# Kernel tuning notes

Measured on AMD Instinct MI355X. Metric: run time of the kernel, lower is better.

The kernel has to match this reference:

```python
import jax, jax.numpy as jnp
import numpy as np

N_CLASSES = 256
N_AUDIO_CHANS = 1
N_CHANS = 128
N_RES = 128
N_SKIP = 256
N_END = 256
KERNEL = 2
N_LAYERS = 10
N_STACKS = 3
DILATIONS = [2 ** i for _ in range(N_STACKS) for i in range(N_LAYERS)]
L = len(DILATIONS)
DN = ('NCW', 'OIW', 'NCW')


def setup_inputs() -> dict:
    key = jax.random.key(0)
    ks = jax.random.split(key, 16)
    s = 0.05  # small init keeps 30-layer residual stack numerically tame
    inp = {
        'x': jax.random.normal(ks[0], (4, N_AUDIO_CHANS, 16384), jnp.float32),
        'w_shift': jax.random.normal(ks[1], (N_CHANS, N_AUDIO_CHANS, KERNEL), jnp.float32) * s,
        'b_shift': jnp.zeros((N_CHANS,), jnp.float32),
        'conv_w': jax.random.normal(ks[2], (L, 2 * N_RES, N_CHANS, KERNEL), jnp.float32) * s,
        'conv_b': jnp.zeros((L, 2 * N_RES), jnp.float32),
        'res_w': jax.random.normal(ks[3], (L, N_CHANS, N_RES), jnp.float32) * s,
        'res_b': jnp.zeros((L, N_CHANS), jnp.float32),
        'skip_w': jax.random.normal(ks[4], (L, N_SKIP, N_RES), jnp.float32) * s,
        'skip_b': jnp.zeros((L, N_SKIP), jnp.float32),
        'a_w': jax.random.normal(ks[5], (N_END, N_SKIP), jnp.float32) * s,
        'a_b': jnp.zeros((N_END,), jnp.float32),
        'b_w': jax.random.normal(ks[6], (N_CLASSES * N_AUDIO_CHANS, N_END), jnp.float32) * s,
        'b_b': jnp.zeros((N_CLASSES * N_AUDIO_CHANS,), jnp.float32),
    }
    return inp


def _causal_conv(x, w, b, dilation):
    # left-pad by (k-1)*dilation so outputs depend only on past/present
    pad = (w.shape[-1] - 1) * dilation
    xp = jnp.pad(x, ((0, 0), (0, 0), (pad, 0)))
    y = jax.lax.conv_general_dilated(xp, w, window_strides=(1,), padding='VALID',
                                     rhs_dilation=(dilation,), dimension_numbers=DN)
    return y + b[None, :, None]


def reference(x, w_shift, b_shift, conv_w, conv_b, res_w, res_b,
              skip_w, skip_b, a_w, a_b, b_w, b_b):
    N, C, W = x.shape
    # shifted conv: shift input right by one (prepend 0, drop last), then causal conv
    xs = jnp.pad(x, ((0, 0), (0, 0), (1, 0)))[:, :, :-1]
    h = _causal_conv(xs, w_shift, b_shift, 1)  # (N, n_chans, W)

    skips = jnp.zeros((N, N_SKIP, W), h.dtype)
    for l in range(L):
        g = _causal_conv(h, conv_w[l], conv_b[l], DILATIONS[l])  # (N, 2*res, W)
        a, b_gate = jnp.split(g, 2, axis=1)
        gated = a * jax.nn.sigmoid(b_gate)                        # GLU, (N, res, W)
        h = jnp.einsum('or,nrw->now', res_w[l], gated) + res_b[l][None, :, None] + h
        skips = skips + jnp.einsum('or,nrw->now', skip_w[l], gated) + skip_b[l][None, :, None]

    z = jax.nn.relu(skips)
    z = jax.nn.relu(jnp.einsum('os,nsw->now', a_w, z) + a_b[None, :, None])
    logits = jnp.einsum('oe,new->now', b_w, z) + b_b[None, :, None]
    return logits.reshape(N, N_CLASSES, N_AUDIO_CHANS, W)
```

## Files before the change

### kernel.cpp

```cpp
#include <hip/hip_runtime.h>
#include <math.h>


#define NB 4
#define WLEN 16384
#define C 128
#define S 256
#define NLAYERS 30
#define TT 64
#define NTB (WLEN / TT)
#define XROW 264
#define GROW 136

typedef _Float16 half8 __attribute__((ext_vector_type(8)));
typedef _Float16 half4 __attribute__((ext_vector_type(4)));
typedef float floatx4 __attribute__((ext_vector_type(4)));

__device__ __forceinline__ float sigmoidf_(float v) {
    return 1.0f / (1.0f + __expf(-v));
}

__global__ void prep_kernel(const float* __restrict__ conv_w,
                            const float* __restrict__ res_w,
                            const float* __restrict__ skip_w,
                            const float* __restrict__ a_w,
                            const float* __restrict__ b_w,
                            const float* __restrict__ conv_b,
                            const float* __restrict__ skip_b,
                            _Float16* __restrict__ cw,
                            _Float16* __restrict__ rsw,
                            _Float16* __restrict__ skw,
                            _Float16* __restrict__ aw,
                            _Float16* __restrict__ bw,
                            float* __restrict__ cbp,
                            float* __restrict__ ssum) {
    const int ncw = NLAYERS * 256 * 256;
    const int nrs = NLAYERS * 128 * 128;
    const int nsk = NLAYERS * 256 * 128;
    const int nab = 256 * 256;
    const int ncb = NLAYERS * 256;
    const int total = ncw + nrs + nsk + nab + nab + ncb + 256;
    for (int idx = blockIdx.x * blockDim.x + threadIdx.x; idx < total;
         idx += gridDim.x * blockDim.x) {
        int i = idx;
        if (i < ncw) {
            int j = i & 7, lane = (i >> 3) & 63, rest = i >> 9;
            int ks = rest & 7; rest >>= 3;
            int mt = rest & 15; int l = rest >> 4;
            int mp = mt * 16 + (lane & 15);
            int orow = (mp >> 1) + (mp & 1) * 128;
            int k = ks * 32 + (lane >> 4) * 8 + j;
            int tap = k >> 7, c = k & 127;
            cw[i] = (_Float16)conv_w[(((size_t)l * 256 + orow) * 128 + c) * 2 + tap];
        } else if (i < ncw + nrs) {
            i -= ncw;
            int j = i & 7, lane = (i >> 3) & 63, rest = i >> 9;
            int ks = rest & 3; rest >>= 2;
            int mt = rest & 7; int l = rest >> 3;
            int m = mt * 16 + (lane & 15);
            int k = ks * 32 + (lane >> 4) * 8 + j;
            rsw[i] = (_Float16)res_w[((size_t)l * 128 + m) * 128 + k];
        } else if (i < ncw + nrs + nsk) {
            i -= ncw + nrs;
            int j = i & 7, lane = (i >> 3) & 63, rest = i >> 9;
            int ks = rest & 3; rest >>= 2;
            int mt = rest & 15; int l = rest >> 4;
            int m = mt * 16 + (lane & 15);
            int k = ks * 32 + (lane >> 4) * 8 + j;
            skw[i] = (_Float16)skip_w[((size_t)l * 256 + m) * 128 + k];
        } else if (i < ncw + nrs + nsk + nab) {
            i -= ncw + nrs + nsk;
            int j = i & 7, lane = (i >> 3) & 63, rest = i >> 9;
            int ks = rest & 7; int mt = rest >> 3;
            aw[i] = (_Float16)a_w[(mt * 16 + (lane & 15)) * 256 + ks * 32 + (lane >> 4) * 8 + j];
        } else if (i < ncw + nrs + nsk + 2 * nab) {
            i -= ncw + nrs + nsk + nab;
            int j = i & 7, lane = (i >> 3) & 63, rest = i >> 9;
            int ks = rest & 7; int mt = rest >> 3;
            bw[i] = (_Float16)b_w[(mt * 16 + (lane & 15)) * 256 + ks * 32 + (lane >> 4) * 8 + j];
        } else if (i < ncw + nrs + nsk + 2 * nab + ncb) {
            i -= ncw + nrs + nsk + 2 * nab;
            int mp = i & 255; int l = i >> 8;
            cbp[i] = conv_b[l * 256 + (mp >> 1) + (mp & 1) * 128];
        } else {
            i -= ncw + nrs + nsk + 2 * nab + ncb;
            float s = 0.f;
            for (int l = 0; l < NLAYERS; ++l) s += skip_b[l * 256 + i];
            ssum[i] = s;
        }
    }
}

__global__ void front_kernel(const float* __restrict__ x,
                             const float* __restrict__ w_shift,
                             const float* __restrict__ b_shift,
                             _Float16* __restrict__ h) {
    const int n = blockIdx.y;
    const int t = blockIdx.x * 256 + threadIdx.x;
    float x1 = (t >= 1) ? x[n * WLEN + t - 1] : 0.0f;
    float x2 = (t >= 2) ? x[n * WLEN + t - 2] : 0.0f;
    _Float16* hq = h + ((size_t)n * WLEN + t) * 128;
    #pragma unroll
    for (int c0 = 0; c0 < 128; c0 += 8) {
        half8 v;
        #pragma unroll
        for (int j = 0; j < 8; ++j) {
            int c = c0 + j;
            v[j] = (_Float16)fmaf(w_shift[2 * c], x2,
                                  fmaf(w_shift[2 * c + 1], x1, b_shift[c]));
        }
        *(half8*)&hq[c0] = v;
    }
}

template <bool FIRST>
__global__ __launch_bounds__(256, 4) void layer_kernel(
    const _Float16* __restrict__ h_in, _Float16* __restrict__ h_out,
    _Float16* __restrict__ chunk,
    const _Float16* __restrict__ cw, const float* __restrict__ cb,
    const _Float16* __restrict__ rsw, const float* __restrict__ rb,
    const _Float16* __restrict__ skw, const float* __restrict__ ssum, int d) {
    __shared__ _Float16 SMEM[2 * TT * GROW];
    _Float16* X0 = SMEM;
    _Float16* X1 = SMEM + TT * GROW;
    _Float16* G  = X0;
    const int n = blockIdx.y, tb = blockIdx.x, t0 = tb * TT;
    const int tid = threadIdx.x;
    const int wave = __builtin_amdgcn_readfirstlane(tid >> 6);
    const int lane = tid & 63, q = lane >> 4, ml = lane & 15;

    const _Float16* hn = h_in + (size_t)n * WLEN * 128;
    #pragma unroll
    for (int it = 0; it < 8; ++it) {
        int idx = it * 256 + tid;
        int seg = idx & 15;
        int rowc = (idx >> 4) & 63;
        int tap = idx >> 10;
        int src_t = t0 + rowc - (tap ? 0 : d);
        half8 v = (half8)(_Float16)0.0f;
        if (src_t >= 0)
            v = *(const half8*)&hn[(size_t)src_t * 128 + seg * 8];
        _Float16* Xb = tap ? X1 : X0;
        *(half8*)&Xb[rowc * GROW + seg * 8] = v;
    }
    __syncthreads();

    floatx4 acc[4][4];
    #pragma unroll
    for (int mt = 0; mt < 4; ++mt)
        #pragma unroll
        for (int r = 0; r < 4; ++r) {
            float bias = cb[64 * wave + mt * 16 + q * 4 + r];
            #pragma unroll
            for (int nt = 0; nt < 4; ++nt) acc[mt][nt][r] = bias;
        }
    #pragma unroll
    for (int half = 0; half < 2; ++half) {
        const _Float16* Xb = half ? X1 : X0;
        for (int ks = 0; ks < 4; ++ks) {
            half8 b[4];
            #pragma unroll
            for (int nt = 0; nt < 4; ++nt)
                b[nt] = *(const half8*)&Xb[(nt * 16 + ml) * GROW + ks * 32 + q * 8];
            #pragma unroll
            for (int mt = 0; mt < 4; ++mt) {
                half8 a = *(const half8*)&cw[((((4 * wave + mt) * 8) + half * 4 + ks) * 64 + lane) * 8];
                #pragma unroll
                for (int nt = 0; nt < 4; ++nt)
                    acc[mt][nt] = __builtin_amdgcn_mfma_f32_16x16x32_f16(a, b[nt], acc[mt][nt], 0, 0, 0);
            }
        }
    }
    __syncthreads();

    #pragma unroll
    for (int mt = 0; mt < 4; ++mt)
        #pragma unroll
        for (int nt = 0; nt < 4; ++nt) {
            float g0 = acc[mt][nt][0] * sigmoidf_(acc[mt][nt][1]);
            float g1 = acc[mt][nt][2] * sigmoidf_(acc[mt][nt][3]);
            _Float16 p[2] = {(_Float16)g0, (_Float16)g1};
            *(uint32_t*)&G[(nt * 16 + ml) * GROW + 32 * wave + mt * 8 + 2 * q] = *(uint32_t*)p;
        }
    __syncthreads();

    {
        floatx4 sacc[4][4];
        #pragma unroll
        for (int mt = 0; mt < 4; ++mt)
            #pragma unroll
            for (int r = 0; r < 4; ++r) {
                float bias = FIRST ? ssum[64 * wave + mt * 16 + q * 4 + r] : 0.0f;
                #pragma unroll
                for (int nt = 0; nt < 4; ++nt) sacc[mt][nt][r] = bias;
            }
        #pragma unroll
        for (int ks = 0; ks < 4; ++ks) {
            half8 b[4];
            #pragma unroll
            for (int nt = 0; nt < 4; ++nt)
                b[nt] = *(const half8*)&G[(nt * 16 + ml) * GROW + ks * 32 + q * 8];
            #pragma unroll
            for (int mt = 0; mt < 4; ++mt) {
                half8 a = *(const half8*)&skw[((((4 * wave + mt) * 4) + ks) * 64 + lane) * 8];
                #pragma unroll
                for (int nt = 0; nt < 4; ++nt)
                    sacc[mt][nt] = __builtin_amdgcn_mfma_f32_16x16x32_f16(a, b[nt], sacc[mt][nt], 0, 0, 0);
            }
        }
        _Float16* cp = chunk + ((size_t)n * NTB + tb) * 16384;
        #pragma unroll
        for (int mt = 0; mt < 4; ++mt)
            #pragma unroll
            for (int nt = 0; nt < 4; ++nt) {
                size_t o = (size_t)((((wave * 4 + mt) * 4) + nt) * 64 + lane) * 4;
                if (FIRST) {
                    half4 v;
                    #pragma unroll
                    for (int r = 0; r < 4; ++r) v[r] = (_Float16)sacc[mt][nt][r];
                    *(half4*)&cp[o] = v;
                } else {
                    half4 v = *(const half4*)&cp[o];
                    half4 w;
                    #pragma unroll
                    for (int r = 0; r < 4; ++r)
                        w[r] = (_Float16)(sacc[mt][nt][r] + (float)v[r]);
                    *(half4*)&cp[o] = w;
                }
            }
    }

    {
        floatx4 racc[2][4];
        #pragma unroll
        for (int mt = 0; mt < 2; ++mt)
            #pragma unroll
            for (int r = 0; r < 4; ++r) {
                float bias = rb[32 * wave + mt * 16 + q * 4 + r];
                #pragma unroll
                for (int nt = 0; nt < 4; ++nt) racc[mt][nt][r] = bias;
            }
        #pragma unroll
        for (int ks = 0; ks < 4; ++ks) {
            half8 b[4];
            #pragma unroll
            for (int nt = 0; nt < 4; ++nt)
                b[nt] = *(const half8*)&G[(nt * 16 + ml) * GROW + ks * 32 + q * 8];
            #pragma unroll
            for (int mt = 0; mt < 2; ++mt) {
                half8 a = *(const half8*)&rsw[((((2 * wave + mt) * 4) + ks) * 64 + lane) * 8];
                #pragma unroll
                for (int nt = 0; nt < 4; ++nt)
                    racc[mt][nt] = __builtin_amdgcn_mfma_f32_16x16x32_f16(a, b[nt], racc[mt][nt], 0, 0, 0);
            }
        }
        _Float16* ho = h_out + (size_t)n * WLEN * 128;
        #pragma unroll
        for (int mt = 0; mt < 2; ++mt)
            #pragma unroll
            for (int nt = 0; nt < 4; ++nt) {
                int tt = nt * 16 + ml;
                int c = 32 * wave + mt * 16 + q * 4;
                half4 hv = *(const half4*)&X1[tt * GROW + c];
                half4 o;
                #pragma unroll
                for (int r = 0; r < 4; ++r)
                    o[r] = (_Float16)(racc[mt][nt][r] + (float)hv[r]);
                *(half4*)&ho[(size_t)(t0 + tt) * 128 + c] = o;
            }
    }
}

__global__ __launch_bounds__(256, 4) void head_kernel(
    float* __restrict__ out, const _Float16* __restrict__ chunk,
    const _Float16* __restrict__ aw, const float* __restrict__ ab,
    const _Float16* __restrict__ bw, const float* __restrict__ bb) {
    __shared__ _Float16 X[TT * XROW];
    const int n = blockIdx.y, tb = blockIdx.x, t0 = tb * TT;
    const int tid = threadIdx.x;
    const int wave = __builtin_amdgcn_readfirstlane(tid >> 6);
    const int lane = tid & 63, q = lane >> 4, ml = lane & 15;

    {
        const _Float16* cp = chunk + ((size_t)n * NTB + tb) * 16384;
        #pragma unroll
        for (int mt = 0; mt < 4; ++mt)
            #pragma unroll
            for (int nt = 0; nt < 4; ++nt) {
                size_t o = (size_t)((((wave * 4 + mt) * 4) + nt) * 64 + lane) * 4;
                half4 v = *(const half4*)&cp[o];
                half4 z;
                #pragma unroll
                for (int r = 0; r < 4; ++r)
                    z[r] = (_Float16)fmaxf((float)v[r], 0.0f);
                *(half4*)&X[(nt * 16 + ml) * XROW + 64 * wave + mt * 16 + q * 4] = z;
            }
    }
    __syncthreads();

    floatx4 acc[4][4];
    #pragma unroll
    for (int mt = 0; mt < 4; ++mt)
        #pragma unroll
        for (int r = 0; r < 4; ++r) {
            float bias = ab[64 * wave + mt * 16 + q * 4 + r];
            #pragma unroll
            for (int nt = 0; nt < 4; ++nt) acc[mt][nt][r] = bias;
        }
    for (int ks = 0; ks < 8; ++ks) {
        half8 b[4];
        #pragma unroll
        for (int nt = 0; nt < 4; ++nt)
            b[nt] = *(const half8*)&X[(nt * 16 + ml) * XROW + ks * 32 + q * 8];
        #pragma unroll
        for (int mt = 0; mt < 4; ++mt) {
            half8 a = *(const half8*)&aw[((((4 * wave + mt) * 8) + ks) * 64 + lane) * 8];
            #pragma unroll
            for (int nt = 0; nt < 4; ++nt)
                acc[mt][nt] = __builtin_amdgcn_mfma_f32_16x16x32_f16(a, b[nt], acc[mt][nt], 0, 0, 0);
        }
    }
    __syncthreads();
    #pragma unroll
    for (int mt = 0; mt < 4; ++mt)
        #pragma unroll
        for (int nt = 0; nt < 4; ++nt) {
            half4 z;
            #pragma unroll
            for (int r = 0; r < 4; ++r)
                z[r] = (_Float16)fmaxf(acc[mt][nt][r], 0.0f);
            *(half4*)&X[(nt * 16 + ml) * XROW + 64 * wave + mt * 16 + q * 4] = z;
        }
    __syncthreads();

    #pragma unroll
    for (int mt = 0; mt < 4; ++mt)
        #pragma unroll
        for (int r = 0; r < 4; ++r) {
            float bias = bb[64 * wave + mt * 16 + q * 4 + r];
            #pragma unroll
            for (int nt = 0; nt < 4; ++nt) acc[mt][nt][r] = bias;
        }
    for (int ks = 0; ks < 8; ++ks) {
        half8 b[4];
        #pragma unroll
        for (int nt = 0; nt < 4; ++nt)
            b[nt] = *(const half8*)&X[(nt * 16 + ml) * XROW + ks * 32 + q * 8];
        #pragma unroll
        for (int mt = 0; mt < 4; ++mt) {
            half8 a = *(const half8*)&bw[((((4 * wave + mt) * 8) + ks) * 64 + lane) * 8];
            #pragma unroll
            for (int nt = 0; nt < 4; ++nt)
                acc[mt][nt] = __builtin_amdgcn_mfma_f32_16x16x32_f16(a, b[nt], acc[mt][nt], 0, 0, 0);
        }
    }
    float* on = out + (size_t)n * S * WLEN;
    #pragma unroll
    for (int mt = 0; mt < 4; ++mt)
        #pragma unroll
        for (int nt = 0; nt < 4; ++nt)
            #pragma unroll
            for (int r = 0; r < 4; ++r) {
                int o = 64 * wave + mt * 16 + q * 4 + r;
                int tt = t0 + nt * 16 + ml;
                on[(size_t)o * WLEN + tt] = acc[mt][nt][r];
            }
}

extern "C" void kernel_launch(void* const* d_in, const int* in_sizes, int n_in,
                              void* d_out, int out_size, void* d_ws, size_t ws_size,
                              hipStream_t stream) {
    (void)in_sizes; (void)n_in; (void)out_size; (void)ws_size;
    const float* x       = (const float*)d_in[0];
    const float* w_shift = (const float*)d_in[1];
    const float* b_shift = (const float*)d_in[2];
    const float* conv_w  = (const float*)d_in[3];
    const float* conv_b  = (const float*)d_in[4];
    const float* res_w   = (const float*)d_in[5];
    const float* res_b   = (const float*)d_in[6];
    const float* skip_w  = (const float*)d_in[7];
    const float* skip_b  = (const float*)d_in[8];
    const float* a_w     = (const float*)d_in[9];
    const float* a_b     = (const float*)d_in[10];
    const float* b_w     = (const float*)d_in[11];
    const float* b_b     = (const float*)d_in[12];
    float* out = (float*)d_out;

    char* ws = (char*)d_ws;
    size_t off = 0;
    _Float16* hA    = (_Float16*)(ws + off); off += (size_t)NB * WLEN * 128 * 2;
    _Float16* hB    = (_Float16*)(ws + off); off += (size_t)NB * WLEN * 128 * 2;
    _Float16* chunk = (_Float16*)(ws + off); off += (size_t)NB * NTB * 16384 * 2;
    _Float16* cw  = (_Float16*)(ws + off); off += (size_t)NLAYERS * 256 * 256 * 2;
    _Float16* rsw = (_Float16*)(ws + off); off += (size_t)NLAYERS * 128 * 128 * 2;
    _Float16* skw = (_Float16*)(ws + off); off += (size_t)NLAYERS * 256 * 128 * 2;
    _Float16* aw  = (_Float16*)(ws + off); off += 256 * 256 * 2;
    _Float16* bw  = (_Float16*)(ws + off); off += 256 * 256 * 2;
    float* cbp  = (float*)(ws + off); off += (size_t)NLAYERS * 256 * 4;
    float* ssum = (float*)(ws + off); off += 256 * 4;

    prep_kernel<<<512, 256, 0, stream>>>(conv_w, res_w, skip_w, a_w, b_w,
                                         conv_b, skip_b,
                                         cw, rsw, skw, aw, bw, cbp, ssum);
    front_kernel<<<dim3(WLEN / 256, NB), 256, 0, stream>>>(x, w_shift, b_shift, hA);

    const dim3 grid(NTB, NB);
    _Float16* hin = hA;
    _Float16* hout = hB;
    for (int l = 0; l < NLAYERS; ++l) {
        int dil = 1 << (l % 10);
        const _Float16* cwp = cw + (size_t)l * 65536;
        const _Float16* rsp = rsw + (size_t)l * 16384;
        const _Float16* skp = skw + (size_t)l * 32768;
        if (l == 0)
            layer_kernel<true><<<grid, 256, 0, stream>>>(
                hin, hout, chunk, cwp, cbp + l * 256,
                rsp, res_b + l * 128, skp, ssum, dil);
        else
            layer_kernel<false><<<grid, 256, 0, stream>>>(
                hin, hout, chunk, cwp, cbp + l * 256,
                rsp, res_b + l * 128, skp, ssum, dil);
        _Float16* tmp = hin; hin = hout; hout = tmp;
    }

    head_kernel<<<grid, 256, 0, stream>>>(out, chunk, aw, a_b, bw, b_b);
}
```

Baseline: 1.150 ms.

## Fuse all WaveNet layers and head into one persistent cooperative kernel

Replaces the 30 per-layer launches and the head launch with a single cooperative kernel that loops over layers and uses a grid-wide sync between them. Skip accumulators stay in registers as fp16 across layers, so the chunk buffer round-trip through global memory is no longer needed. The head is fused at the end. The cost is a grid barrier per layer, higher register pressure from the persistent skip state, and fp16 rounding of the skip sum after every layer. If the occupancy check fails, the old multi-kernel path is used instead.

```diff
diff --git a/kernel.cpp b/kernel.cpp
--- a/kernel.cpp
+++ b/kernel.cpp
@@ -1,5 +1,8 @@
 #include <hip/hip_runtime.h>
+#include <hip/hip_cooperative_groups.h>
 #include <math.h>
+
+namespace cg = cooperative_groups;
 
 
 #define NB 4
@@ -113,6 +116,272 @@
     }
 }
 
+__global__ __launch_bounds__(256, 4) void wavenet_coop(
+    _Float16* __restrict__ hA, _Float16* __restrict__ hB,
+    float* __restrict__ out,
+    const _Float16* __restrict__ cw_all, const float* __restrict__ cbp_all,
+    const _Float16* __restrict__ rsw_all, const float* __restrict__ rb_all,
+    const _Float16* __restrict__ skw_all, const float* __restrict__ ssum,
+    const _Float16* __restrict__ aw, const float* __restrict__ ab,
+    const _Float16* __restrict__ bw, const float* __restrict__ bb) {
+    __shared__ _Float16 SMEM[2 * TT * GROW];
+    _Float16* X0 = SMEM;
+    _Float16* X1 = SMEM + TT * GROW;
+    _Float16* G  = X0;
+    cg::grid_group gg = cg::this_grid();
+    const int n = blockIdx.y, tb = blockIdx.x, t0 = tb * TT;
+    const int tid = threadIdx.x;
+    const int wave = __builtin_amdgcn_readfirstlane(tid >> 6);
+    const int lane = tid & 63, q = lane >> 4, ml = lane & 15;
+
+    half4 sk16[4][4];
+
+    #pragma clang loop unroll(disable)
+    for (int l = 0; l < NLAYERS; ++l) {
+        const _Float16* hin = (l & 1) ? hB : hA;
+        _Float16* hout      = (l & 1) ? hA : hB;
+        const int d = 1 << (l % 10);
+        const _Float16* cw  = cw_all  + (size_t)l * 65536;
+        const float*    cb  = cbp_all + l * 256;
+        const _Float16* rsw = rsw_all + (size_t)l * 16384;
+        const float*    rb  = rb_all  + l * 128;
+        const _Float16* skw = skw_all + (size_t)l * 32768;
+
+        const _Float16* hn = hin + (size_t)n * WLEN * 128;
+        #pragma unroll
+        for (int it = 0; it < 8; ++it) {
+            int idx = it * 256 + tid;
+            int seg = idx & 15;
+            int rowc = (idx >> 4) & 63;
+            int tap = idx >> 10;
+            int src_t = t0 + rowc - (tap ? 0 : d);
+            half8 v = (half8)(_Float16)0.0f;
+            if (src_t >= 0)
+                v = *(const half8*)&hn[(size_t)src_t * 128 + seg * 8];
+            _Float16* Xb = tap ? X1 : X0;
+            *(half8*)&Xb[rowc * GROW + seg * 8] = v;
+        }
+        __syncthreads();
+
+        uint32_t glu[4][4];
+        #pragma unroll
+        for (int mp2 = 0; mp2 < 2; ++mp2) {
+            floatx4 acc[2][4];
+            #pragma unroll
+            for (int i = 0; i < 2; ++i) {
+                int mt = 2 * mp2 + i;
+                #pragma unroll
+                for (int r = 0; r < 4; ++r) {
+                    float bias = cb[64 * wave + mt * 16 + q * 4 + r];
+                    #pragma unroll
+                    for (int nt = 0; nt < 4; ++nt) acc[i][nt][r] = bias;
+                }
+            }
+            #pragma unroll
+            for (int hp = 0; hp < 2; ++hp) {
+                const _Float16* Xb = hp ? X1 : X0;
+                for (int ks = 0; ks < 4; ++ks) {
+                    half8 b[4];
+                    #pragma unroll
+                    for (int nt = 0; nt < 4; ++nt)
+                        b[nt] = *(const half8*)&Xb[(nt * 16 + ml) * GROW + ks * 32 + q * 8];
+                    #pragma unroll
+                    for (int i = 0; i < 2; ++i) {
+                        int mt = 2 * mp2 + i;
+                        half8 a = *(const half8*)&cw[((((4 * wave + mt) * 8) + hp * 4 + ks) * 64 + lane) * 8];
+                        #pragma unroll
+                        for (int nt = 0; nt < 4; ++nt)
+                            acc[i][nt] = __builtin_amdgcn_mfma_f32_16x16x32_f16(a, b[nt], acc[i][nt], 0, 0, 0);
+                    }
+                }
+            }
+            #pragma unroll
+            for (int i = 0; i < 2; ++i)
+                #pragma unroll
+                for (int nt = 0; nt < 4; ++nt) {
+                    float g0 = acc[i][nt][0] * sigmoidf_(acc[i][nt][1]);
+                    float g1 = acc[i][nt][2] * sigmoidf_(acc[i][nt][3]);
+                    _Float16 p[2] = {(_Float16)g0, (_Float16)g1};
+                    glu[2 * mp2 + i][nt] = *(uint32_t*)p;
+                }
+        }
+        __syncthreads();
+        #pragma unroll
+        for (int mt = 0; mt < 4; ++mt)
+            #pragma unroll
+            for (int nt = 0; nt < 4; ++nt)
+                *(uint32_t*)&G[(nt * 16 + ml) * GROW + 32 * wave + mt * 8 + 2 * q] = glu[mt][nt];
+        __syncthreads();
+
+        {
+            floatx4 sacc[4][4];
+            if (l == 0) {
+                #pragma unroll
+                for (int mt = 0; mt < 4; ++mt)
+                    #pragma unroll
+                    for (int r = 0; r < 4; ++r) {
+                        float bias = ssum[64 * wave + mt * 16 + q * 4 + r];
+                        #pragma unroll
+                        for (int nt = 0; nt < 4; ++nt) sacc[mt][nt][r] = bias;
+                    }
+            } else {
+                #pragma unroll
+                for (int mt = 0; mt < 4; ++mt)
+                    #pragma unroll
+                    for (int nt = 0; nt < 4; ++nt)
+                        #pragma unroll
+                        for (int r = 0; r < 4; ++r)
+                            sacc[mt][nt][r] = (float)sk16[mt][nt][r];
+            }
+            #pragma unroll
+            for (int ks = 0; ks < 4; ++ks) {
+                half8 b[4];
+                #pragma unroll
+                for (int nt = 0; nt < 4; ++nt)
+                    b[nt] = *(const half8*)&G[(nt * 16 + ml) * GROW + ks * 32 + q * 8];
+                #pragma unroll
+                for (int mt = 0; mt < 4; ++mt) {
+                    half8 a = *(const half8*)&skw[((((4 * wave + mt) * 4) + ks) * 64 + lane) * 8];
+                    #pragma unroll
+                    for (int nt = 0; nt < 4; ++nt)
+                        sacc[mt][nt] = __builtin_amdgcn_mfma_f32_16x16x32_f16(a, b[nt], sacc[mt][nt], 0, 0, 0);
+                }
+            }
+            #pragma unroll
+            for (int mt = 0; mt < 4; ++mt)
+                #pragma unroll
+                for (int nt = 0; nt < 4; ++nt)
+                    #pragma unroll
+                    for (int r = 0; r < 4; ++r)
+                        sk16[mt][nt][r] = (_Float16)sacc[mt][nt][r];
+        }
+
+        if (l != NLAYERS - 1) {
+            floatx4 racc[2][4];
+            #pragma unroll
+            for (int mt = 0; mt < 2; ++mt)
+                #pragma unroll
+                for (int r = 0; r < 4; ++r) {
+                    float bias = rb[32 * wave + mt * 16 + q * 4 + r];
+                    #pragma unroll
+                    for (int nt = 0; nt < 4; ++nt) racc[mt][nt][r] = bias;
+                }
+            #pragma unroll
+            for (int ks = 0; ks < 4; ++ks) {
+                half8 b[4];
+                #pragma unroll
+                for (int nt = 0; nt < 4; ++nt)
+                    b[nt] = *(const half8*)&G[(nt * 16 + ml) * GROW + ks * 32 + q * 8];
+                #pragma unroll
+                for (int mt = 0; mt < 2; ++mt) {
+                    half8 a = *(const half8*)&rsw[((((2 * wave + mt) * 4) + ks) * 64 + lane) * 8];
+                    #pragma unroll
+                    for (int nt = 0; nt < 4; ++nt)
+                        racc[mt][nt] = __builtin_amdgcn_mfma_f32_16x16x32_f16(a, b[nt], racc[mt][nt], 0, 0, 0);
+                }
+            }
+            _Float16* ho = hout + (size_t)n * WLEN * 128;
+            #pragma unroll
+            for (int mt = 0; mt < 2; ++mt)
+                #pragma unroll
+                for (int nt = 0; nt < 4; ++nt) {
+                    int tt = nt * 16 + ml;
+                    int c = 32 * wave + mt * 16 + q * 4;
+                    half4 hv = *(const half4*)&X1[tt * GROW + c];
+                    half4 o;
+                    #pragma unroll
+                    for (int r = 0; r < 4; ++r)
+                        o[r] = (_Float16)(racc[mt][nt][r] + (float)hv[r]);
+                    *(half4*)&ho[(size_t)(t0 + tt) * 128 + c] = o;
+                }
+            gg.sync();
+        }
+    }
+
+    __syncthreads();
+    _Float16* X = SMEM;
+    #pragma unroll
+    for (int mt = 0; mt < 4; ++mt)
+        #pragma unroll
+        for (int nt = 0; nt < 4; ++nt) {
+            half4 v = sk16[mt][nt];
+            half4 z;
+            #pragma unroll
+            for (int r = 0; r < 4; ++r)
+                z[r] = (_Float16)fmaxf((float)v[r], 0.0f);
+            *(half4*)&X[(nt * 16 + ml) * XROW + 64 * wave + mt * 16 + q * 4] = z;
+        }
+    __syncthreads();
+
+    floatx4 acc[4][4];
+    #pragma unroll
+    for (int mt = 0; mt < 4; ++mt)
+        #pragma unroll
+        for (int r = 0; r < 4; ++r) {
+            float bias = ab[64 * wave + mt * 16 + q * 4 + r];
+            #pragma unroll
+            for (int nt = 0; nt < 4; ++nt) acc[mt][nt][r] = bias;
+        }
+    for (int ks = 0; ks < 8; ++ks) {
+        half8 b[4];
+        #pragma unroll
+        for (int nt = 0; nt < 4; ++nt)
+            b[nt] = *(const half8*)&X[(nt * 16 + ml) * XROW + ks * 32 + q * 8];
+        #pragma unroll
+        for (int mt = 0; mt < 4; ++mt) {
+            half8 a = *(const half8*)&aw[((((4 * wave + mt) * 8) + ks) * 64 + lane) * 8];
+            #pragma unroll
+            for (int nt = 0; nt < 4; ++nt)
+                acc[mt][nt] = __builtin_amdgcn_mfma_f32_16x16x32_f16(a, b[nt], acc[mt][nt], 0, 0, 0);
+        }
+    }
+    __syncthreads();
+    #pragma unroll
+    for (int mt = 0; mt < 4; ++mt)
+        #pragma unroll
+        for (int nt = 0; nt < 4; ++nt) {
+            half4 z;
+            #pragma unroll
+            for (int r = 0; r < 4; ++r)
+                z[r] = (_Float16)fmaxf(acc[mt][nt][r], 0.0f);
+            *(half4*)&X[(nt * 16 + ml) * XROW + 64 * wave + mt * 16 + q * 4] = z;
+        }
+    __syncthreads();
+
+    #pragma unroll
+    for (int mt = 0; mt < 4; ++mt)
+        #pragma unroll
+        for (int r = 0; r < 4; ++r) {
+            float bias = bb[64 * wave + mt * 16 + q * 4 + r];
+            #pragma unroll
+            for (int nt = 0; nt < 4; ++nt) acc[mt][nt][r] = bias;
+        }
+    for (int ks = 0; ks < 8; ++ks) {
+        half8 b[4];
+        #pragma unroll
+        for (int nt = 0; nt < 4; ++nt)
+            b[nt] = *(const half8*)&X[(nt * 16 + ml) * XROW + ks * 32 + q * 8];
+        #pragma unroll
+        for (int mt = 0; mt < 4; ++mt) {
+            half8 a = *(const half8*)&bw[((((4 * wave + mt) * 8) + ks) * 64 + lane) * 8];
+            #pragma unroll
+            for (int nt = 0; nt < 4; ++nt)
+                acc[mt][nt] = __builtin_amdgcn_mfma_f32_16x16x32_f16(a, b[nt], acc[mt][nt], 0, 0, 0);
+        }
+    }
+    float* on = out + (size_t)n * S * WLEN;
+    #pragma unroll
+    for (int mt = 0; mt < 4; ++mt)
+        #pragma unroll
+        for (int nt = 0; nt < 4; ++nt)
+            #pragma unroll
+            for (int r = 0; r < 4; ++r) {
+                int o = 64 * wave + mt * 16 + q * 4 + r;
+                int tt = t0 + nt * 16 + ml;
+                on[(size_t)o * WLEN + tt] = acc[mt][nt][r];
+            }
+}
+
 template <bool FIRST>
 __global__ __launch_bounds__(256, 4) void layer_kernel(
     const _Float16* __restrict__ h_in, _Float16* __restrict__ h_out,
@@ -155,8 +424,8 @@
             for (int nt = 0; nt < 4; ++nt) acc[mt][nt][r] = bias;
         }
     #pragma unroll
-    for (int half = 0; half < 2; ++half) {
-        const _Float16* Xb = half ? X1 : X0;
+    for (int hp = 0; hp < 2; ++hp) {
+        const _Float16* Xb = hp ? X1 : X0;
         for (int ks = 0; ks < 4; ++ks) {
             half8 b[4];
             #pragma unroll
@@ -164,7 +433,7 @@
                 b[nt] = *(const half8*)&Xb[(nt * 16 + ml) * GROW + ks * 32 + q * 8];
             #pragma unroll
             for (int mt = 0; mt < 4; ++mt) {
-                half8 a = *(const half8*)&cw[((((4 * wave + mt) * 8) + half * 4 + ks) * 64 + lane) * 8];
+                half8 a = *(const half8*)&cw[((((4 * wave + mt) * 8) + hp * 4 + ks) * 64 + lane) * 8];
                 #pragma unroll
                 for (int nt = 0; nt < 4; ++nt)
                     acc[mt][nt] = __builtin_amdgcn_mfma_f32_16x16x32_f16(a, b[nt], acc[mt][nt], 0, 0, 0);
@@ -405,23 +674,42 @@
     front_kernel<<<dim3(WLEN / 256, NB), 256, 0, stream>>>(x, w_shift, b_shift, hA);
 
     const dim3 grid(NTB, NB);
-    _Float16* hin = hA;
-    _Float16* hout = hB;
-    for (int l = 0; l < NLAYERS; ++l) {
-        int dil = 1 << (l % 10);
-        const _Float16* cwp = cw + (size_t)l * 65536;
-        const _Float16* rsp = rsw + (size_t)l * 16384;
-        const _Float16* skp = skw + (size_t)l * 32768;
-        if (l == 0)
-            layer_kernel<true><<<grid, 256, 0, stream>>>(
-                hin, hout, chunk, cwp, cbp + l * 256,
-                rsp, res_b + l * 128, skp, ssum, dil);
-        else
-            layer_kernel<false><<<grid, 256, 0, stream>>>(
-                hin, hout, chunk, cwp, cbp + l * 256,
-                rsp, res_b + l * 128, skp, ssum, dil);
-        _Float16* tmp = hin; hin = hout; hout = tmp;
-    }
-
-    head_kernel<<<grid, 256, 0, stream>>>(out, chunk, aw, a_b, bw, b_b);
+
+    static int coop_blocks_per_cu = -1;
+    if (coop_blocks_per_cu < 0) {
+        int nb = 0;
+        if (hipOccupancyMaxActiveBlocksPerMultiprocessor(&nb, wavenet_coop, 256, 0)
+            != hipSuccess)
+            nb = 0;
+        coop_blocks_per_cu = nb;
+    }
+
+    bool launched = false;
+    if (coop_blocks_per_cu >= 4) {
+        void* args[] = {&hA, &hB, &out, &cw, &cbp, &rsw, (void*)&res_b,
+                        &skw, &ssum, &aw, (void*)&a_b, &bw, (void*)&b_b};
+        launched = hipLaunchCooperativeKernel((const void*)wavenet_coop, grid,
+                                              dim3(256), args, 0, stream) == hipSuccess;
+    }
+
+    if (!launched) {
+        _Float16* hin = hA;
+        _Float16* hout = hB;
+        for (int l = 0; l < NLAYERS; ++l) {
+            int dil = 1 << (l % 10);
+            const _Float16* cwp = cw + (size_t)l * 65536;
+            const _Float16* rsp = rsw + (size_t)l * 16384;
+            const _Float16* skp = skw + (size_t)l * 32768;
+            if (l == 0)
+                layer_kernel<true><<<grid, 256, 0, stream>>>(
+                    hin, hout, chunk, cwp, cbp + l * 256,
+                    rsp, res_b + l * 128, skp, ssum, dil);
+            else
+                layer_kernel<false><<<grid, 256, 0, stream>>>(
+                    hin, hout, chunk, cwp, cbp + l * 256,
+                    rsp, res_b + l * 128, skp, ssum, dil);
+            _Float16* tmp = hin; hin = hout; hout = tmp;
+        }
+        head_kernel<<<grid, 256, 0, stream>>>(out, chunk, aw, a_b, bw, b_b);
+    }
 }
```

Result: no change. 1.151 ms (+0.0%).

## Use 512-thread blocks with 8 waves splitting output rows in layer and head kernels

Applied to the files above, without the earlier changes.

Doubles the block size to 8 waves. Each wave now computes half as many output-channel tiles in the gated conv, skip, residual and head GEMMs, which cuts accumulator registers per thread and the launch bounds now ask for 8 blocks per CU to raise occupancy. Loop order is flipped so A fragments are held in registers and B is reloaded per n-tile. The cost is more LDS reads per MFMA, since every wave reloads the full B tiles, and with 2*TT*GROW half shared memory per block, reaching 8 blocks per CU may be limited by LDS.

```diff
diff --git a/kernel.cpp b/kernel.cpp
--- a/kernel.cpp
+++ b/kernel.cpp
@@ -114,7 +114,7 @@
 }
 
 template <bool FIRST>
-__global__ __launch_bounds__(256, 4) void layer_kernel(
+__global__ __launch_bounds__(512, 8) void layer_kernel(
     const _Float16* __restrict__ h_in, _Float16* __restrict__ h_out,
     _Float16* __restrict__ chunk,
     const _Float16* __restrict__ cw, const float* __restrict__ cb,
@@ -131,8 +131,8 @@
 
     const _Float16* hn = h_in + (size_t)n * WLEN * 128;
     #pragma unroll
-    for (int it = 0; it < 8; ++it) {
-        int idx = it * 256 + tid;
+    for (int it = 0; it < 4; ++it) {
+        int idx = it * 512 + tid;
         int seg = idx & 15;
         int rowc = (idx >> 4) & 63;
         int tap = idx >> 10;
@@ -145,75 +145,75 @@
     }
     __syncthreads();
 
-    floatx4 acc[4][4];
-    #pragma unroll
-    for (int mt = 0; mt < 4; ++mt)
+    floatx4 acc[2][4];
+    #pragma unroll
+    for (int mt = 0; mt < 2; ++mt)
         #pragma unroll
         for (int r = 0; r < 4; ++r) {
-            float bias = cb[64 * wave + mt * 16 + q * 4 + r];
+            float bias = cb[32 * wave + mt * 16 + q * 4 + r];
             #pragma unroll
             for (int nt = 0; nt < 4; ++nt) acc[mt][nt][r] = bias;
         }
     #pragma unroll
-    for (int half = 0; half < 2; ++half) {
-        const _Float16* Xb = half ? X1 : X0;
+    for (int hp = 0; hp < 2; ++hp) {
+        const _Float16* Xb = hp ? X1 : X0;
         for (int ks = 0; ks < 4; ++ks) {
-            half8 b[4];
-            #pragma unroll
-            for (int nt = 0; nt < 4; ++nt)
-                b[nt] = *(const half8*)&Xb[(nt * 16 + ml) * GROW + ks * 32 + q * 8];
-            #pragma unroll
-            for (int mt = 0; mt < 4; ++mt) {
-                half8 a = *(const half8*)&cw[((((4 * wave + mt) * 8) + half * 4 + ks) * 64 + lane) * 8];
+            half8 a[2];
+            #pragma unroll
+            for (int mt = 0; mt < 2; ++mt)
+                a[mt] = *(const half8*)&cw[((((2 * wave + mt) * 8) + hp * 4 + ks) * 64 + lane) * 8];
+            #pragma unroll
+            for (int nt = 0; nt < 4; ++nt) {
+                half8 b = *(const half8*)&Xb[(nt * 16 + ml) * GROW + ks * 32 + q * 8];
                 #pragma unroll
-                for (int nt = 0; nt < 4; ++nt)
-                    acc[mt][nt] = __builtin_amdgcn_mfma_f32_16x16x32_f16(a, b[nt], acc[mt][nt], 0, 0, 0);
-            }
-        }
-    }
-    __syncthreads();
-
-    #pragma unroll
-    for (int mt = 0; mt < 4; ++mt)
+                for (int mt = 0; mt < 2; ++mt)
+                    acc[mt][nt] = __builtin_amdgcn_mfma_f32_16x16x32_f16(a[mt], b, acc[mt][nt], 0, 0, 0);
+            }
+        }
+    }
+    __syncthreads();
+
+    #pragma unroll
+    for (int mt = 0; mt < 2; ++mt)
         #pragma unroll
         for (int nt = 0; nt < 4; ++nt) {
             float g0 = acc[mt][nt][0] * sigmoidf_(acc[mt][nt][1]);
             float g1 = acc[mt][nt][2] * sigmoidf_(acc[mt][nt][3]);
             _Float16 p[2] = {(_Float16)g0, (_Float16)g1};
-            *(uint32_t*)&G[(nt * 16 + ml) * GROW + 32 * wave + mt * 8 + 2 * q] = *(uint32_t*)p;
+            *(uint32_t*)&G[(nt * 16 + ml) * GROW + 16 * wave + mt * 8 + 2 * q] = *(uint32_t*)p;
         }
     __syncthreads();
 
     {
-        floatx4 sacc[4][4];
-        #pragma unroll
-        for (int mt = 0; mt < 4; ++mt)
+        floatx4 sacc[2][4];
+        #pragma unroll
+        for (int mt = 0; mt < 2; ++mt)
             #pragma unroll
             for (int r = 0; r < 4; ++r) {
-                float bias = FIRST ? ssum[64 * wave + mt * 16 + q * 4 + r] : 0.0f;
+                float bias = FIRST ? ssum[32 * wave + mt * 16 + q * 4 + r] : 0.0f;
                 #pragma unroll
                 for (int nt = 0; nt < 4; ++nt) sacc[mt][nt][r] = bias;
             }
         #pragma unroll
         for (int ks = 0; ks < 4; ++ks) {
-            half8 b[4];
-            #pragma unroll
-            for (int nt = 0; nt < 4; ++nt)
-                b[nt] = *(const half8*)&G[(nt * 16 + ml) * GROW + ks * 32 + q * 8];
-            #pragma unroll
-            for (int mt = 0; mt < 4; ++mt) {
-                half8 a = *(const half8*)&skw[((((4 * wave + mt) * 4) + ks) * 64 + lane) * 8];
+            half8 a[2];
+            #pragma unroll
+            for (int mt = 0; mt < 2; ++mt)
+                a[mt] = *(const half8*)&skw[((((2 * wave + mt) * 4) + ks) * 64 + lane) * 8];
+            #pragma unroll
+            for (int nt = 0; nt < 4; ++nt) {
+                half8 b = *(const half8*)&G[(nt * 16 + ml) * GROW + ks * 32 + q * 8];
                 #pragma unroll
-                for (int nt = 0; nt < 4; ++nt)
-                    sacc[mt][nt] = __builtin_amdgcn_mfma_f32_16x16x32_f16(a, b[nt], sacc[mt][nt], 0, 0, 0);
+                for (int mt = 0; mt < 2; ++mt)
+                    sacc[mt][nt] = __builtin_amdgcn_mfma_f32_16x16x32_f16(a[mt], b, sacc[mt][nt], 0, 0, 0);
             }
         }
         _Float16* cp = chunk + ((size_t)n * NTB + tb) * 16384;
         #pragma unroll
-        for (int mt = 0; mt < 4; ++mt)
+        for (int mt = 0; mt < 2; ++mt)
             #pragma unroll
             for (int nt = 0; nt < 4; ++nt) {
-                size_t o = (size_t)((((wave * 4 + mt) * 4) + nt) * 64 + lane) * 4;
+                size_t o = (size_t)((((wave * 2 + mt) * 4) + nt) * 64 + lane) * 4;
                 if (FIRST) {
                     half4 v;
                     #pragma unroll
@@ -231,47 +231,38 @@
     }
 
     {
-        floatx4 racc[2][4];
-        #pragma unroll
-        for (int mt = 0; mt < 2; ++mt)
-            #pragma unroll
-            for (int r = 0; r < 4; ++r) {
-                float bias = rb[32 * wave + mt * 16 + q * 4 + r];
-                #pragma unroll
-                for (int nt = 0; nt < 4; ++nt) racc[mt][nt][r] = bias;
-            }
+        floatx4 racc[4];
+        #pragma unroll
+        for (int r = 0; r < 4; ++r) {
+            float bias = rb[16 * wave + q * 4 + r];
+            #pragma unroll
+            for (int nt = 0; nt < 4; ++nt) racc[nt][r] = bias;
+        }
         #pragma unroll
         for (int ks = 0; ks < 4; ++ks) {
-            half8 b[4];
-            #pragma unroll
-            for (int nt = 0; nt < 4; ++nt)
-                b[nt] = *(const half8*)&G[(nt * 16 + ml) * GROW + ks * 32 + q * 8];
-            #pragma unroll
-            for (int mt = 0; mt < 2; ++mt) {
-                half8 a = *(const half8*)&rsw[((((2 * wave + mt) * 4) + ks) * 64 + lane) * 8];
-                #pragma unroll
-                for (int nt = 0; nt < 4; ++nt)
-                    racc[mt][nt] = __builtin_amdgcn_mfma_f32_16x16x32_f16(a, b[nt], racc[mt][nt], 0, 0, 0);
+            half8 a = *(const half8*)&rsw[(((wave * 4) + ks) * 64 + lane) * 8];
+            #pragma unroll
+            for (int nt = 0; nt < 4; ++nt) {
+                half8 b = *(const half8*)&G[(nt * 16 + ml) * GROW + ks * 32 + q * 8];
+                racc[nt] = __builtin_amdgcn_mfma_f32_16x16x32_f16(a, b, racc[nt], 0, 0, 0);
             }
         }
         _Float16* ho = h_out + (size_t)n * WLEN * 128;
         #pragma unroll
-        for (int mt = 0; mt < 2; ++mt)
-            #pragma unroll
-            for (int nt = 0; nt < 4; ++nt) {
-                int tt = nt * 16 + ml;
-                int c = 32 * wave + mt * 16 + q * 4;
-                half4 hv = *(const half4*)&X1[tt * GROW + c];
-                half4 o;
-                #pragma unroll
-                for (int r = 0; r < 4; ++r)
-                    o[r] = (_Float16)(racc[mt][nt][r] + (float)hv[r]);
-                *(half4*)&ho[(size_t)(t0 + tt) * 128 + c] = o;
-            }
-    }
-}
-
-__global__ __launch_bounds__(256, 4) void head_kernel(
+        for (int nt = 0; nt < 4; ++nt) {
+            int tt = nt * 16 + ml;
+            int c = 16 * wave + q * 4;
+            half4 hv = *(const half4*)&X1[tt * GROW + c];
+            half4 o;
+            #pragma unroll
+            for (int r = 0; r < 4; ++r)
+                o[r] = (_Float16)(racc[nt][r] + (float)hv[r]);
+            *(half4*)&ho[(size_t)(t0 + tt) * 128 + c] = o;
+        }
+    }
+}
+
+__global__ __launch_bounds__(512, 8) void head_kernel(
     float* __restrict__ out, const _Float16* __restrict__ chunk,
     const _Float16* __restrict__ aw, const float* __restrict__ ab,
     const _Float16* __restrict__ bw, const float* __restrict__ bb) {
@@ -284,84 +275,84 @@
     {
         const _Float16* cp = chunk + ((size_t)n * NTB + tb) * 16384;
         #pragma unroll
-        for (int mt = 0; mt < 4; ++mt)
+        for (int mt = 0; mt < 2; ++mt)
             #pragma unroll
             for (int nt = 0; nt < 4; ++nt) {
-                size_t o = (size_t)((((wave * 4 + mt) * 4) + nt) * 64 + lane) * 4;
+                size_t o = (size_t)((((wave * 2 + mt) * 4) + nt) * 64 + lane) * 4;
                 half4 v = *(const half4*)&cp[o];
                 half4 z;
                 #pragma unroll
                 for (int r = 0; r < 4; ++r)
                     z[r] = (_Float16)fmaxf((float)v[r], 0.0f);
-                *(half4*)&X[(nt * 16 + ml) * XROW + 64 * wave + mt * 16 + q * 4] = z;
-            }
-    }
-    __syncthreads();
-
-    floatx4 acc[4][4];
-    #pragma unroll
-    for (int mt = 0; mt < 4; ++mt)
+                *(half4*)&X[(nt * 16 + ml) * XROW + 32 * wave + mt * 16 + q * 4] = z;
+            }
+    }
+    __syncthreads();
+
+    floatx4 acc[2][4];
+    #pragma unroll
+    for (int mt = 0; mt < 2; ++mt)
         #pragma unroll
         for (int r = 0; r < 4; ++r) {
-            float bias = ab[64 * wave + mt * 16 + q * 4 + r];
+            float bias = ab[32 * wave + mt * 16 + q * 4 + r];
             #pragma unroll
             for (int nt = 0; nt < 4; ++nt) acc[mt][nt][r] = bias;
         }
     for (int ks = 0; ks < 8; ++ks) {
-        half8 b[4];
-        #pragma unroll
-        for (int nt = 0; nt < 4; ++nt)
-            b[nt] = *(const half8*)&X[(nt * 16 + ml) * XROW + ks * 32 + q * 8];
-        #pragma unroll
-        for (int mt = 0; mt < 4; ++mt) {
-            half8 a = *(const half8*)&aw[((((4 * wave + mt) * 8) + ks) * 64 + lane) * 8];
-            #pragma unroll
-            for (int nt = 0; nt < 4; ++nt)
-                acc[mt][nt] = __builtin_amdgcn_mfma_f32_16x16x32_f16(a, b[nt], acc[mt][nt], 0, 0, 0);
-        }
-    }
-    __syncthreads();
-    #pragma unroll
-    for (int mt = 0; mt < 4; ++mt)
+        half8 a[2];
+        #pragma unroll
+        for (int mt = 0; mt < 2; ++mt)
+            a[mt] = *(const half8*)&aw[((((2 * wave + mt) * 8) + ks) * 64 + lane) * 8];
+        #pragma unroll
+        for (int nt = 0; nt < 4; ++nt) {
+            half8 b = *(const half8*)&X[(nt * 16 + ml) * XROW + ks * 32 + q * 8];
+            #pragma unroll
+            for (int mt = 0; mt < 2; ++mt)
+                acc[mt][nt] = __builtin_amdgcn_mfma_f32_16x16x32_f16(a[mt], b, acc[mt][nt], 0, 0, 0);
+        }
+    }
+    __syncthreads();
+    #pragma unroll
+    for (int mt = 0; mt < 2; ++mt)
         #pragma unroll
         for (int nt = 0; nt < 4; ++nt) {
             half4 z;
             #pragma unroll
             for (int r = 0; r < 4; ++r)
                 z[r] = (_Float16)fmaxf(acc[mt][nt][r], 0.0f);
-            *(half4*)&X[(nt * 16 + ml) * XROW + 64 * wave + mt * 16 + q * 4] = z;
-        }
-    __syncthreads();
-
-    #pragma unroll
-    for (int mt = 0; mt < 4; ++mt)
+            *(half4*)&X[(nt * 16 + ml) * XROW + 32 * wave + mt * 16 + q * 4] = z;
+        }
+    __syncthreads();
+
+    #pragma unroll
+    for (int mt = 0; mt < 2; ++mt)
         #pragma unroll
         for (int r = 0; r < 4; ++r) {
-            float bias = bb[64 * wave + mt * 16 + q * 4 + r];
+            float bias = bb[32 * wave + mt * 16 + q * 4 + r];
             #pragma unroll
             for (int nt = 0; nt < 4; ++nt) acc[mt][nt][r] = bias;
         }
     for (int ks = 0; ks < 8; ++ks) {
-        half8 b[4];
+        half8 a[2];
+        #pragma unroll
+        for (int mt = 0; mt < 2; ++mt)
+            a[mt] = *(const half8*)&bw[((((2 * wave + mt) * 8) + ks) * 64 + lane) * 8];
+        #pragma unroll
+        for (int nt = 0; nt < 4; ++nt) {
+            half8 b = *(const half8*)&X[(nt * 16 + ml) * XROW + ks * 32 + q * 8];
+            #pragma unroll
+            for (int mt = 0; mt < 2; ++mt)
+                acc[mt][nt] = __builtin_amdgcn_mfma_f32_16x16x32_f16(a[mt], b, acc[mt][nt], 0, 0, 0);
+        }
+    }
+    float* on = out + (size_t)n * S * WLEN;
+    #pragma unroll
+    for (int mt = 0; mt < 2; ++mt)
         #pragma unroll
         for (int nt = 0; nt < 4; ++nt)
-            b[nt] = *(const half8*)&X[(nt * 16 + ml) * XROW + ks * 32 + q * 8];
-        #pragma unroll
-        for (int mt = 0; mt < 4; ++mt) {
-            half8 a = *(const half8*)&bw[((((4 * wave + mt) * 8) + ks) * 64 + lane) * 8];
-            #pragma unroll
-            for (int nt = 0; nt < 4; ++nt)
-                acc[mt][nt] = __builtin_amdgcn_mfma_f32_16x16x32_f16(a, b[nt], acc[mt][nt], 0, 0, 0);
-        }
-    }
-    float* on = out + (size_t)n * S * WLEN;
-    #pragma unroll
-    for (int mt = 0; mt < 4; ++mt)
-        #pragma unroll
-        for (int nt = 0; nt < 4; ++nt)
             #pragma unroll
             for (int r = 0; r < 4; ++r) {
-                int o = 64 * wave + mt * 16 + q * 4 + r;
+                int o = 32 * wave + mt * 16 + q * 4 + r;
                 int tt = t0 + nt * 16 + ml;
                 on[(size_t)o * WLEN + tt] = acc[mt][nt][r];
             }
@@ -413,15 +404,15 @@
         const _Float16* rsp = rsw + (size_t)l * 16384;
         const _Float16* skp = skw + (size_t)l * 32768;
         if (l == 0)
-            layer_kernel<true><<<grid, 256, 0, stream>>>(
+            layer_kernel<true><<<grid, 512, 0, stream>>>(
                 hin, hout, chunk, cwp, cbp + l * 256,
                 rsp, res_b + l * 128, skp, ssum, dil);
         else
-            layer_kernel<false><<<grid, 256, 0, stream>>>(
+            layer_kernel<false><<<grid, 512, 0, stream>>>(
                 hin, hout, chunk, cwp, cbp + l * 256,
                 rsp, res_b + l * 128, skp, ssum, dil);
         _Float16* tmp = hin; hin = hout; hout = tmp;
     }
 
-    head_kernel<<<grid, 256, 0, stream>>>(out, chunk, aw, a_b, bw, b_b);
-}
+    head_kernel<<<grid, 512, 0, stream>>>(out, chunk, aw, a_b, bw, b_b);
+}
```

After: 1.100 ms. 1.05x faster.
